# Optimization experiments

Measured on AMD Instinct MI355X. Metric: run time of the kernel, lower is better.

## Reference

```python
import jax, jax.numpy as jnp
import numpy as np


def setup_inputs() -> dict:
    key = jax.random.key(0)
    k_u, k_a, k_b, k_c, k_d = jax.random.split(key, 5)
    B, T, Din, Dout, S = 16, 4096, 256, 256, 256
    return {
        "u": jax.random.normal(k_u, (B, T, Din), dtype=jnp.float32),
        "a_raw": jnp.zeros((S,), dtype=jnp.float32),
        "b": jax.random.normal(k_b, (S, Din), dtype=jnp.float32) * 0.1,
        "c": jax.random.normal(k_c, (Dout, S), dtype=jnp.float32) * 0.1,
        "d": jax.random.normal(k_d, (Dout, Din), dtype=jnp.float32) * 0.1,
    }


def reference(u, a_raw, b, c, d):
    # u: (B, T, Din) -> y: (B, T, Dout)
    # Recurrence: x_t = a * x_{t-1} + b @ u_t ;  y_t = c @ x_t + d @ u_t
    a = jnp.tanh(a_raw)                                  # (S,)
    Bu = jnp.einsum('btd,sd->bts', u, b)                 # input projection, (B,T,S)

    def step(x, bu_t):
        x = x * a + bu_t                                 # diagonal state update
        return x, x

    x0 = jnp.zeros((u.shape[0], a.shape[0]), dtype=u.dtype)
    _, xs = jax.lax.scan(step, x0, jnp.swapaxes(Bu, 0, 1))  # xs: (T,B,S)
    xs = jnp.swapaxes(xs, 0, 1)                              # (B,T,S)

    y = jnp.einsum('bts,os->bto', xs, c) + jnp.einsum('bti,oi->bto', u, d)
    return y  # dropout(p=0.0) is identity
```

## Files before the change

kernel.cpp:

```cpp
#include <hip/hip_runtime.h>

#define DEV __device__ __forceinline__

typedef unsigned short u16;
typedef __attribute__((ext_vector_type(8))) __bf16 bf16x8;
typedef __attribute__((ext_vector_type(4))) float f32x4;
typedef __attribute__((ext_vector_type(8))) unsigned short u16x8;
typedef __attribute__((ext_vector_type(4))) unsigned short u16x4;

static constexpr int NB = 16;
static constexpr int NT = 4096;
static constexpr int NCH = 64;
static constexpr int LCH = 64;

DEV u16 f2bf(float f) {
  unsigned u = __builtin_bit_cast(unsigned, f);
  u += 0x7fffu + ((u >> 16) & 1u);
  return (u16)(u >> 16);
}
DEV float bf2f(u16 h) {
  unsigned u = ((unsigned)h) << 16;
  return __builtin_bit_cast(float, u);
}

DEV void gl_lds16(const void* gp, void* lp) {
  __builtin_amdgcn_global_load_lds(
      (__attribute__((address_space(1))) void*)(void*)gp,
      (__attribute__((address_space(3))) void*)lp, 16, 0, 0);
}

__global__ __launch_bounds__(256) void prep_k(const float* __restrict__ a_raw,
                                              const float* __restrict__ b,
                                              const float* __restrict__ c,
                                              const float* __restrict__ d,
                                              float* __restrict__ af,
                                              u16* __restrict__ wq,
                                              u16* __restrict__ cw) {
  int i = blockIdx.x * 256 + threadIdx.x;
  if (i < 256) af[i] = tanhf(a_raw[i]);
  wq[i] = f2bf(b[i]);
  wq[65536 + i] = f2bf(d[i]);
  cw[i] = f2bf(c[i]);
}

__global__ __launch_bounds__(1024, 4) void gemm1_k(const float* __restrict__ u,
                                                   const u16* __restrict__ wq,
                                                   const float* __restrict__ af,
                                                   u16* __restrict__ bu,
                                                   u16* __restrict__ ud,
                                                   float* __restrict__ carry) {
  __shared__ u16 As[64 * 64];
  __shared__ u16 Ws[512 * 64];
  const int tid = threadIdx.x;
  const int lane = tid & 63;
  const int wid = tid >> 6;
  const int bx = blockIdx.x;
  const size_t row0 = (size_t)bx * 64;

  const int arow = tid >> 4;
  const int ak = (tid & 15) * 4;
  const int abyte = arow * 128 + ((((tid & 15) >> 1) ^ (arow & 7)) * 16) + (tid & 1) * 8;

  const f32x4 zero = {0.f, 0.f, 0.f, 0.f};
  f32x4 acc[4][2];
#pragma unroll
  for (int i = 0; i < 4; ++i) { acc[i][0] = zero; acc[i][1] = zero; }

#pragma unroll
  for (int kt = 0; kt < 4; ++kt) {
    const int kb = kt * 64;
    float4 av = *reinterpret_cast<const float4*>(u + (row0 + arow) * 256 + kb + ak);
#pragma unroll
    for (int r = 0; r < 4; ++r) {
      int wrow = r * 128 + (tid >> 3);
      int sc = (tid & 7) ^ (wrow & 7);
      gl_lds16(wq + (size_t)wrow * 256 + kb + sc * 8,
               (char*)Ws + r * 16384 + wid * 1024);
    }
    u16x4 a4;
    a4[0] = f2bf(av.x); a4[1] = f2bf(av.y); a4[2] = f2bf(av.z); a4[3] = f2bf(av.w);
    *reinterpret_cast<u16x4*>((char*)As + abyte) = a4;
    __syncthreads();
#pragma unroll
    for (int kk = 0; kk < 2; ++kk) {
      const int ks = kk * 4 + (lane >> 4);
      bf16x8 afr[4], bfr[2];
#pragma unroll
      for (int mi = 0; mi < 4; ++mi) {
        int ar = mi * 16 + (lane & 15);
        afr[mi] = *reinterpret_cast<const bf16x8*>(
            (const char*)As + ar * 128 + ((ks ^ (ar & 7)) * 16));
      }
#pragma unroll
      for (int ni = 0; ni < 2; ++ni) {
        int br = wid * 32 + ni * 16 + (lane & 15);
        bfr[ni] = *reinterpret_cast<const bf16x8*>(
            (const char*)Ws + br * 128 + ((ks ^ (br & 7)) * 16));
      }
#pragma unroll
      for (int mi = 0; mi < 4; ++mi)
#pragma unroll
        for (int ni = 0; ni < 2; ++ni)
          acc[mi][ni] = __builtin_amdgcn_mfma_f32_16x16x32_bf16(
              afr[mi], bfr[ni], acc[mi][ni], 0, 0, 0);
    }
    if (kt < 3) __syncthreads();
  }

#pragma unroll
  for (int mi = 0; mi < 4; ++mi) {
    int rl = mi * 16 + (lane >> 4) * 4;
#pragma unroll
    for (int ni = 0; ni < 2; ++ni) {
      int col = wid * 32 + ni * 16 + (lane & 15);
#pragma unroll
      for (int q = 0; q < 4; ++q) {
        size_t R = row0 + rl + q;
        u16 h = f2bf(acc[mi][ni][q]);
        if (wid < 8)
          bu[R * 256 + (((col >> 3) ^ ((int)R & 7)) * 8) + (col & 7)] = h;
        else
          ud[R * 256 + (col - 256)] = h;
      }
    }
  }

  if (wid < 8) {
    const int tb = (lane >> 4) * 4;
#pragma unroll
    for (int ni = 0; ni < 2; ++ni) {
      int col = wid * 32 + ni * 16 + (lane & 15);
      float a = af[col];
      float c2 = a * a, c4 = c2 * c2, c8 = c4 * c4;
      float a12 = c8 * c4;
      float a13 = a12 * a;
      float base = (tb == 0) ? a12 : (tb == 4) ? c8 : (tb == 8) ? c4 : 1.0f;
      float p = base, s = 0.f;
#pragma unroll
      for (int mi = 3; mi >= 0; --mi) {
#pragma unroll
        for (int q = 3; q >= 0; --q) {
          s = fmaf(p, acc[mi][ni][q], s);
          if (q) p *= a;
        }
        if (mi) p *= a13;
      }
      s += __shfl_xor(s, 16, 64);
      s += __shfl_xor(s, 32, 64);
      if ((lane >> 4) == 0) carry[(size_t)bx * 256 + col] = s;
    }
  }
}

__global__ __launch_bounds__(256) void scan2_k(const float* __restrict__ carry,
                                               const float* __restrict__ af,
                                               float* __restrict__ initb) {
  int b = blockIdx.x;
  int s = threadIdx.x;
  float a = af[s];
  float aL = a;
#pragma unroll
  for (int i = 0; i < 6; ++i) aL *= aL;
  float x = 0.f;
  for (int k = 0; k < NCH; ++k) {
    size_t idx = ((size_t)(b * NCH + k)) * 256 + s;
    float cv = carry[idx];
    initb[idx] = x;
    x = fmaf(aL, x, cv);
  }
}

__global__ __launch_bounds__(512, 4) void gemm2_k(const u16* __restrict__ bu,
                                                  const u16* __restrict__ cw,
                                                  const u16* __restrict__ ud,
                                                  const float* __restrict__ af,
                                                  const float* __restrict__ initb,
                                                  float* __restrict__ y) {
  __shared__ u16 XS[128 * 256];
  __shared__ u16 CS[128 * 64];
  const int tid = threadIdx.x;
  const int lane = tid & 63;
  const int wid = tid >> 6;
  const int wr = wid >> 2, wc = wid & 3;
  const int bx = blockIdx.x;
  const int col0 = blockIdx.y * 128;

  const char* src = (const char*)bu + (size_t)bx * 65536;
#pragma unroll
  for (int j = 0; j < 8; ++j)
    gl_lds16(src + j * 8192 + tid * 16, (char*)XS + j * 8192 + wid * 1024);
#pragma unroll
  for (int r = 0; r < 2; ++r) {
    int brow = r * 64 + (tid >> 3);
    int sc = (tid & 7) ^ (brow & 7);
    gl_lds16(cw + (size_t)(col0 + brow) * 256 + 0 + sc * 8,
             (char*)CS + r * 8192 + wid * 1024);
  }
  __syncthreads();

  {
    const int hf = tid >> 8;
    const int s = tid & 255;
    const float a = af[s];
    float x = initb[(size_t)(bx * 2 + hf) * 256 + s];
    const int r0 = hf * 64;
    const int slot = s >> 3;
    const int off = (s & 7);
#pragma unroll 8
    for (int t = 0; t < 64; ++t) {
      int r = r0 + t;
      int bi = r * 256 + ((slot ^ (r & 7)) * 8) + off;
      x = fmaf(a, x, bf2f(XS[bi]));
      XS[bi] = f2bf(x);
    }
  }

  f32x4 acc[4][2];
#pragma unroll
  for (int mi = 0; mi < 4; ++mi) {
    int rlb = wr * 64 + mi * 16 + (lane >> 4) * 4;
#pragma unroll
    for (int ni = 0; ni < 2; ++ni) {
      int col = col0 + wc * 32 + ni * 16 + (lane & 15);
#pragma unroll
      for (int q = 0; q < 4; ++q)
        acc[mi][ni][q] = bf2f(ud[(size_t)(bx * 128 + rlb + q) * 256 + col]);
    }
  }
  __syncthreads();

#pragma unroll
  for (int kt = 0; kt < 4; ++kt) {
#pragma unroll
    for (int kk = 0; kk < 2; ++kk) {
      const int ksl = kk * 4 + (lane >> 4);
      const int ksg = kt * 8 + ksl;
      bf16x8 afr[4], bfr[2];
#pragma unroll
      for (int mi = 0; mi < 4; ++mi) {
        int ar = wr * 64 + mi * 16 + (lane & 15);
        afr[mi] = *reinterpret_cast<const bf16x8*>(&XS[ar * 256 + ((ksg ^ (ar & 7)) * 8)]);
      }
#pragma unroll
      for (int ni = 0; ni < 2; ++ni) {
        int nr = wc * 32 + ni * 16 + (lane & 15);
        bfr[ni] = *reinterpret_cast<const bf16x8*>(&CS[nr * 64 + ((ksl ^ (nr & 7)) * 8)]);
      }
#pragma unroll
      for (int mi = 0; mi < 4; ++mi)
#pragma unroll
        for (int ni = 0; ni < 2; ++ni)
          acc[mi][ni] = __builtin_amdgcn_mfma_f32_16x16x32_bf16(
              afr[mi], bfr[ni], acc[mi][ni], 0, 0, 0);
    }
    if (kt < 3) {
      __syncthreads();
#pragma unroll
      for (int r = 0; r < 2; ++r) {
        int brow = r * 64 + (tid >> 3);
        int sc = (tid & 7) ^ (brow & 7);
        gl_lds16(cw + (size_t)(col0 + brow) * 256 + (kt + 1) * 64 + sc * 8,
                 (char*)CS + r * 8192 + wid * 1024);
      }
      __syncthreads();
    }
  }

#pragma unroll
  for (int mi = 0; mi < 4; ++mi) {
    int rlb = wr * 64 + mi * 16 + (lane >> 4) * 4;
#pragma unroll
    for (int ni = 0; ni < 2; ++ni) {
      int col = col0 + wc * 32 + ni * 16 + (lane & 15);
#pragma unroll
      for (int q = 0; q < 4; ++q)
        y[(size_t)(bx * 128 + rlb + q) * 256 + col] = acc[mi][ni][q];
    }
  }
}

extern "C" void kernel_launch(void* const* d_in, const int* in_sizes, int n_in,
                              void* d_out, int out_size, void* d_ws, size_t ws_size,
                              hipStream_t stream) {
  const float* u = (const float*)d_in[0];
  const float* a_raw = (const float*)d_in[1];
  const float* b = (const float*)d_in[2];
  const float* c = (const float*)d_in[3];
  const float* d = (const float*)d_in[4];
  float* y = (float*)d_out;
  char* ws = (char*)d_ws;

  const size_t MB = 1u << 20;
  float* af = (float*)(ws);
  u16* wq = (u16*)(ws + 65536);
  u16* cw = (u16*)(ws + 65536 + 262144);
  u16* bu = (u16*)(ws + 1 * MB);
  u16* ud = (u16*)(ws + 33 * MB);
  float* carry = (float*)(ws + 65 * MB);
  float* initb = (float*)(ws + 66 * MB);

  prep_k<<<256, 256, 0, stream>>>(a_raw, b, c, d, af, wq, cw);
  gemm1_k<<<1024, 1024, 0, stream>>>(u, wq, af, bu, ud, carry);
  scan2_k<<<16, 256, 0, stream>>>(carry, af, initb);
  gemm2_k<<<dim3(512, 2), 512, 0, stream>>>(bu, cw, ud, af, initb, y);
}
```

Measured before the change: 90.71 us.

## Split gemm1 into 4 column panels per chunk, loading operands directly without LDS

```diff
diff --git a/kernel.cpp b/kernel.cpp
--- a/kernel.cpp
+++ b/kernel.cpp
@@ -27,6 +27,13 @@
   __builtin_amdgcn_global_load_lds(
       (__attribute__((address_space(1))) void*)(void*)gp,
       (__attribute__((address_space(3))) void*)lp, 16, 0, 0);
+}
+
+DEV bf16x8 cvt8(float4 a, float4 b) {
+  u16x8 o;
+  o[0] = f2bf(a.x); o[1] = f2bf(a.y); o[2] = f2bf(a.z); o[3] = f2bf(a.w);
+  o[4] = f2bf(b.x); o[5] = f2bf(b.y); o[6] = f2bf(b.z); o[7] = f2bf(b.w);
+  return __builtin_bit_cast(bf16x8, o);
 }
 
 __global__ __launch_bounds__(256) void prep_k(const float* __restrict__ a_raw,
@@ -43,68 +50,57 @@
   cw[i] = f2bf(c[i]);
 }
 
-__global__ __launch_bounds__(1024, 4) void gemm1_k(const float* __restrict__ u,
-                                                   const u16* __restrict__ wq,
-                                                   const float* __restrict__ af,
-                                                   u16* __restrict__ bu,
-                                                   u16* __restrict__ ud,
-                                                   float* __restrict__ carry) {
-  __shared__ u16 As[64 * 64];
-  __shared__ u16 Ws[512 * 64];
+__global__ __launch_bounds__(256, 3) void gemm1_k(const float* __restrict__ u,
+                                                  const u16* __restrict__ wq,
+                                                  const float* __restrict__ af,
+                                                  u16* __restrict__ bu,
+                                                  u16* __restrict__ ud,
+                                                  float* __restrict__ carry) {
   const int tid = threadIdx.x;
   const int lane = tid & 63;
   const int wid = tid >> 6;
   const int bx = blockIdx.x;
-  const size_t row0 = (size_t)bx * 64;
-
-  const int arow = tid >> 4;
-  const int ak = (tid & 15) * 4;
-  const int abyte = arow * 128 + ((((tid & 15) >> 1) ^ (arow & 7)) * 16) + (tid & 1) * 8;
+  const int chunk = bx >> 2;
+  const int panel = bx & 3;
+  const size_t row0 = (size_t)chunk * 64;
+
+  const int lr = lane & 15;
+  const int lk = (lane >> 4) * 8;
 
   const f32x4 zero = {0.f, 0.f, 0.f, 0.f};
   f32x4 acc[4][2];
 #pragma unroll
   for (int i = 0; i < 4; ++i) { acc[i][0] = zero; acc[i][1] = zero; }
 
+  const float* ubase = u + (row0 + lr) * 256 + lk;
+  const u16* wbase = wq + (size_t)(panel * 128 + wid * 32 + lr) * 256 + lk;
+
 #pragma unroll
   for (int kt = 0; kt < 4; ++kt) {
-    const int kb = kt * 64;
-    float4 av = *reinterpret_cast<const float4*>(u + (row0 + arow) * 256 + kb + ak);
-#pragma unroll
-    for (int r = 0; r < 4; ++r) {
-      int wrow = r * 128 + (tid >> 3);
-      int sc = (tid & 7) ^ (wrow & 7);
-      gl_lds16(wq + (size_t)wrow * 256 + kb + sc * 8,
-               (char*)Ws + r * 16384 + wid * 1024);
-    }
-    u16x4 a4;
-    a4[0] = f2bf(av.x); a4[1] = f2bf(av.y); a4[2] = f2bf(av.z); a4[3] = f2bf(av.w);
-    *reinterpret_cast<u16x4*>((char*)As + abyte) = a4;
-    __syncthreads();
-#pragma unroll
-    for (int kk = 0; kk < 2; ++kk) {
-      const int ks = kk * 4 + (lane >> 4);
-      bf16x8 afr[4], bfr[2];
+#pragma unroll
+    for (int ks = 0; ks < 2; ++ks) {
+      const int k = kt * 64 + ks * 32;
+      float4 a0[4], a1[4];
 #pragma unroll
       for (int mi = 0; mi < 4; ++mi) {
-        int ar = mi * 16 + (lane & 15);
-        afr[mi] = *reinterpret_cast<const bf16x8*>(
-            (const char*)As + ar * 128 + ((ks ^ (ar & 7)) * 16));
-      }
-#pragma unroll
-      for (int ni = 0; ni < 2; ++ni) {
-        int br = wid * 32 + ni * 16 + (lane & 15);
-        bfr[ni] = *reinterpret_cast<const bf16x8*>(
-            (const char*)Ws + br * 128 + ((ks ^ (br & 7)) * 16));
-      }
+        const float* p = ubase + (size_t)mi * 16 * 256 + k;
+        a0[mi] = *reinterpret_cast<const float4*>(p);
+        a1[mi] = *reinterpret_cast<const float4*>(p + 4);
+      }
+      bf16x8 bf[2];
+#pragma unroll
+      for (int ni = 0; ni < 2; ++ni)
+        bf[ni] = *reinterpret_cast<const bf16x8*>(wbase + (size_t)ni * 16 * 256 + k);
+      bf16x8 afr[4];
+#pragma unroll
+      for (int mi = 0; mi < 4; ++mi) afr[mi] = cvt8(a0[mi], a1[mi]);
 #pragma unroll
       for (int mi = 0; mi < 4; ++mi)
 #pragma unroll
         for (int ni = 0; ni < 2; ++ni)
           acc[mi][ni] = __builtin_amdgcn_mfma_f32_16x16x32_bf16(
-              afr[mi], bfr[ni], acc[mi][ni], 0, 0, 0);
-    }
-    if (kt < 3) __syncthreads();
+              afr[mi], bf[ni], acc[mi][ni], 0, 0, 0);
+    }
   }
 
 #pragma unroll
@@ -112,12 +108,12 @@
     int rl = mi * 16 + (lane >> 4) * 4;
 #pragma unroll
     for (int ni = 0; ni < 2; ++ni) {
-      int col = wid * 32 + ni * 16 + (lane & 15);
+      int col = panel * 128 + wid * 32 + ni * 16 + lr;
 #pragma unroll
       for (int q = 0; q < 4; ++q) {
         size_t R = row0 + rl + q;
         u16 h = f2bf(acc[mi][ni][q]);
-        if (wid < 8)
+        if (panel < 2)
           bu[R * 256 + (((col >> 3) ^ ((int)R & 7)) * 8) + (col & 7)] = h;
         else
           ud[R * 256 + (col - 256)] = h;
@@ -125,11 +121,11 @@
     }
   }
 
-  if (wid < 8) {
+  if (panel < 2) {
     const int tb = (lane >> 4) * 4;
 #pragma unroll
     for (int ni = 0; ni < 2; ++ni) {
-      int col = wid * 32 + ni * 16 + (lane & 15);
+      int col = panel * 128 + wid * 32 + ni * 16 + lr;
       float a = af[col];
       float c2 = a * a, c4 = c2 * c2, c8 = c4 * c4;
       float a12 = c8 * c4;
@@ -147,7 +143,7 @@
       }
       s += __shfl_xor(s, 16, 64);
       s += __shfl_xor(s, 32, 64);
-      if ((lane >> 4) == 0) carry[(size_t)bx * 256 + col] = s;
+      if ((lane >> 4) == 0) carry[(size_t)chunk * 256 + col] = s;
     }
   }
 }
@@ -300,7 +296,7 @@
   float* initb = (float*)(ws + 66 * MB);
 
   prep_k<<<256, 256, 0, stream>>>(a_raw, b, c, d, af, wq, cw);
-  gemm1_k<<<1024, 1024, 0, stream>>>(u, wq, af, bu, ud, carry);
+  gemm1_k<<<4096, 256, 0, stream>>>(u, wq, af, bu, ud, carry);
   scan2_k<<<16, 256, 0, stream>>>(carry, af, initb);
   gemm2_k<<<dim3(512, 2), 512, 0, stream>>>(bu, cw, ud, af, initb, y);
 }
```

Result: slower. 200.4 us (+120.9%).

## Convert u to bf16 once and move the D projection into gemm2

Applied to the files above, without the earlier changes.

```diff
diff --git a/kernel.cpp b/kernel.cpp
--- a/kernel.cpp
+++ b/kernel.cpp
@@ -34,73 +34,83 @@
                                               const float* __restrict__ c,
                                               const float* __restrict__ d,
                                               float* __restrict__ af,
-                                              u16* __restrict__ wq,
-                                              u16* __restrict__ cw) {
+                                              u16* __restrict__ bw,
+                                              u16* __restrict__ cw,
+                                              u16* __restrict__ dw) {
   int i = blockIdx.x * 256 + threadIdx.x;
   if (i < 256) af[i] = tanhf(a_raw[i]);
-  wq[i] = f2bf(b[i]);
-  wq[65536 + i] = f2bf(d[i]);
+  bw[i] = f2bf(b[i]);
   cw[i] = f2bf(c[i]);
-}
-
-__global__ __launch_bounds__(1024, 4) void gemm1_k(const float* __restrict__ u,
-                                                   const u16* __restrict__ wq,
-                                                   const float* __restrict__ af,
-                                                   u16* __restrict__ bu,
-                                                   u16* __restrict__ ud,
-                                                   float* __restrict__ carry) {
-  __shared__ u16 As[64 * 64];
-  __shared__ u16 Ws[512 * 64];
+  dw[i] = f2bf(d[i]);
+}
+
+__global__ __launch_bounds__(256) void convu_k(const float* __restrict__ u,
+                                               u16* __restrict__ ub) {
+  size_t i = ((size_t)blockIdx.x * 256 + threadIdx.x) * 8;
+  float4 v0 = *reinterpret_cast<const float4*>(u + i);
+  float4 v1 = *reinterpret_cast<const float4*>(u + i + 4);
+  u16x8 o;
+  o[0] = f2bf(v0.x); o[1] = f2bf(v0.y); o[2] = f2bf(v0.z); o[3] = f2bf(v0.w);
+  o[4] = f2bf(v1.x); o[5] = f2bf(v1.y); o[6] = f2bf(v1.z); o[7] = f2bf(v1.w);
+  *reinterpret_cast<u16x8*>(ub + i) = o;
+}
+
+__global__ __launch_bounds__(256) void gemm1_k(const u16* __restrict__ ubf,
+                                               const u16* __restrict__ bw,
+                                               const float* __restrict__ af,
+                                               u16* __restrict__ bu,
+                                               float* __restrict__ carry) {
+  __shared__ u16 As[128 * 64];
+  __shared__ u16 Bs[128 * 64];
   const int tid = threadIdx.x;
   const int lane = tid & 63;
   const int wid = tid >> 6;
-  const int bx = blockIdx.x;
-  const size_t row0 = (size_t)bx * 64;
-
-  const int arow = tid >> 4;
-  const int ak = (tid & 15) * 4;
-  const int abyte = arow * 128 + ((((tid & 15) >> 1) ^ (arow & 7)) * 16) + (tid & 1) * 8;
+  const int wm = wid >> 1, wn = wid & 1;
+  const int panel = blockIdx.x;
+  const size_t row0 = (size_t)blockIdx.y * 128;
+  const int col0 = panel * 128;
+
+  const int rstg = tid >> 3;
+  const int c16 = tid & 7;
 
   const f32x4 zero = {0.f, 0.f, 0.f, 0.f};
-  f32x4 acc[4][2];
-#pragma unroll
-  for (int i = 0; i < 4; ++i) { acc[i][0] = zero; acc[i][1] = zero; }
+  f32x4 acc[4][4];
+#pragma unroll
+  for (int i = 0; i < 4; ++i)
+#pragma unroll
+    for (int j = 0; j < 4; ++j) acc[i][j] = zero;
 
 #pragma unroll
   for (int kt = 0; kt < 4; ++kt) {
     const int kb = kt * 64;
-    float4 av = *reinterpret_cast<const float4*>(u + (row0 + arow) * 256 + kb + ak);
-#pragma unroll
-    for (int r = 0; r < 4; ++r) {
-      int wrow = r * 128 + (tid >> 3);
-      int sc = (tid & 7) ^ (wrow & 7);
-      gl_lds16(wq + (size_t)wrow * 256 + kb + sc * 8,
-               (char*)Ws + r * 16384 + wid * 1024);
-    }
-    u16x4 a4;
-    a4[0] = f2bf(av.x); a4[1] = f2bf(av.y); a4[2] = f2bf(av.z); a4[3] = f2bf(av.w);
-    *reinterpret_cast<u16x4*>((char*)As + abyte) = a4;
+#pragma unroll
+    for (int j = 0; j < 4; ++j) {
+      int row = j * 32 + rstg;
+      int sc = c16 ^ (row & 7);
+      gl_lds16(ubf + (row0 + row) * 256 + kb + sc * 8,
+               (char*)As + j * 4096 + wid * 1024);
+      gl_lds16(bw + (size_t)(col0 + row) * 256 + kb + sc * 8,
+               (char*)Bs + j * 4096 + wid * 1024);
+    }
     __syncthreads();
 #pragma unroll
     for (int kk = 0; kk < 2; ++kk) {
       const int ks = kk * 4 + (lane >> 4);
-      bf16x8 afr[4], bfr[2];
+      bf16x8 afr[4], bfr[4];
 #pragma unroll
       for (int mi = 0; mi < 4; ++mi) {
-        int ar = mi * 16 + (lane & 15);
-        afr[mi] = *reinterpret_cast<const bf16x8*>(
-            (const char*)As + ar * 128 + ((ks ^ (ar & 7)) * 16));
-      }
-#pragma unroll
-      for (int ni = 0; ni < 2; ++ni) {
-        int br = wid * 32 + ni * 16 + (lane & 15);
-        bfr[ni] = *reinterpret_cast<const bf16x8*>(
-            (const char*)Ws + br * 128 + ((ks ^ (br & 7)) * 16));
+        int ar = wm * 64 + mi * 16 + (lane & 15);
+        afr[mi] = *reinterpret_cast<const bf16x8*>(&As[ar * 64 + (ks ^ (ar & 7)) * 8]);
+      }
+#pragma unroll
+      for (int ni = 0; ni < 4; ++ni) {
+        int br = wn * 64 + ni * 16 + (lane & 15);
+        bfr[ni] = *reinterpret_cast<const bf16x8*>(&Bs[br * 64 + (ks ^ (br & 7)) * 8]);
       }
 #pragma unroll
       for (int mi = 0; mi < 4; ++mi)
 #pragma unroll
-        for (int ni = 0; ni < 2; ++ni)
+        for (int ni = 0; ni < 4; ++ni)
           acc[mi][ni] = __builtin_amdgcn_mfma_f32_16x16x32_bf16(
               afr[mi], bfr[ni], acc[mi][ni], 0, 0, 0);
     }
@@ -109,27 +119,24 @@
 
 #pragma unroll
   for (int mi = 0; mi < 4; ++mi) {
-    int rl = mi * 16 + (lane >> 4) * 4;
-#pragma unroll
-    for (int ni = 0; ni < 2; ++ni) {
-      int col = wid * 32 + ni * 16 + (lane & 15);
+    int rl = wm * 64 + mi * 16 + (lane >> 4) * 4;
+#pragma unroll
+    for (int ni = 0; ni < 4; ++ni) {
+      int col = col0 + wn * 64 + ni * 16 + (lane & 15);
 #pragma unroll
       for (int q = 0; q < 4; ++q) {
         size_t R = row0 + rl + q;
-        u16 h = f2bf(acc[mi][ni][q]);
-        if (wid < 8)
-          bu[R * 256 + (((col >> 3) ^ ((int)R & 7)) * 8) + (col & 7)] = h;
-        else
-          ud[R * 256 + (col - 256)] = h;
-      }
-    }
-  }
-
-  if (wid < 8) {
+        bu[R * 256 + (((col >> 3) ^ ((int)R & 7)) * 8) + (col & 7)] = f2bf(acc[mi][ni][q]);
+      }
+    }
+  }
+
+  {
+    const int chunk = (int)(blockIdx.y) * 2 + wm;
     const int tb = (lane >> 4) * 4;
 #pragma unroll
-    for (int ni = 0; ni < 2; ++ni) {
-      int col = wid * 32 + ni * 16 + (lane & 15);
+    for (int ni = 0; ni < 4; ++ni) {
+      int col = col0 + wn * 64 + ni * 16 + (lane & 15);
       float a = af[col];
       float c2 = a * a, c4 = c2 * c2, c8 = c4 * c4;
       float a12 = c8 * c4;
@@ -147,7 +154,7 @@
       }
       s += __shfl_xor(s, 16, 64);
       s += __shfl_xor(s, 32, 64);
-      if ((lane >> 4) == 0) carry[(size_t)bx * 256 + col] = s;
+      if ((lane >> 4) == 0) carry[(size_t)chunk * 256 + col] = s;
     }
   }
 }
@@ -172,7 +179,8 @@
 
 __global__ __launch_bounds__(512, 4) void gemm2_k(const u16* __restrict__ bu,
                                                   const u16* __restrict__ cw,
-                                                  const u16* __restrict__ ud,
+                                                  const u16* __restrict__ dw,
+                                                  const u16* __restrict__ ubf,
                                                   const float* __restrict__ af,
                                                   const float* __restrict__ initb,
                                                   float* __restrict__ y) {
@@ -182,8 +190,8 @@
   const int lane = tid & 63;
   const int wid = tid >> 6;
   const int wr = wid >> 2, wc = wid & 3;
-  const int bx = blockIdx.x;
-  const int col0 = blockIdx.y * 128;
+  const int bx = blockIdx.y;
+  const int col0 = blockIdx.x * 128;
 
   const char* src = (const char*)bu + (size_t)bx * 65536;
 #pragma unroll
@@ -216,17 +224,9 @@
   }
 
   f32x4 acc[4][2];
-#pragma unroll
-  for (int mi = 0; mi < 4; ++mi) {
-    int rlb = wr * 64 + mi * 16 + (lane >> 4) * 4;
-#pragma unroll
-    for (int ni = 0; ni < 2; ++ni) {
-      int col = col0 + wc * 32 + ni * 16 + (lane & 15);
-#pragma unroll
-      for (int q = 0; q < 4; ++q)
-        acc[mi][ni][q] = bf2f(ud[(size_t)(bx * 128 + rlb + q) * 256 + col]);
-    }
-  }
+  const f32x4 zero = {0.f, 0.f, 0.f, 0.f};
+#pragma unroll
+  for (int mi = 0; mi < 4; ++mi) { acc[mi][0] = zero; acc[mi][1] = zero; }
   __syncthreads();
 
 #pragma unroll
@@ -263,6 +263,48 @@
                  (char*)CS + r * 8192 + wid * 1024);
       }
       __syncthreads();
+    }
+  }
+
+#pragma unroll
+  for (int kt = 0; kt < 4; ++kt) {
+    __syncthreads();
+#pragma unroll
+    for (int j = 0; j < 2; ++j) {
+      int row = j * 64 + (tid >> 3);
+      int sc = (tid & 7) ^ (row & 7);
+      gl_lds16(ubf + ((size_t)bx * 128 + row) * 256 + kt * 64 + sc * 8,
+               (char*)XS + j * 8192 + wid * 1024);
+    }
+#pragma unroll
+    for (int r = 0; r < 2; ++r) {
+      int brow = r * 64 + (tid >> 3);
+      int sc = (tid & 7) ^ (brow & 7);
+      gl_lds16(dw + (size_t)(col0 + brow) * 256 + kt * 64 + sc * 8,
+               (char*)CS + r * 8192 + wid * 1024);
+    }
+    __syncthreads();
+#pragma unroll
+    for (int kk = 0; kk < 2; ++kk) {
+      const int ksl = kk * 4 + (lane >> 4);
+      bf16x8 afr[4], bfr[2];
+#pragma unroll
+      for (int mi = 0; mi < 4; ++mi) {
+        int ar = wr * 64 + mi * 16 + (lane & 15);
+        afr[mi] = *reinterpret_cast<const bf16x8*>(
+            (const char*)XS + ar * 128 + ((ksl ^ (ar & 7)) * 16));
+      }
+#pragma unroll
+      for (int ni = 0; ni < 2; ++ni) {
+        int nr = wc * 32 + ni * 16 + (lane & 15);
+        bfr[ni] = *reinterpret_cast<const bf16x8*>(&CS[nr * 64 + ((ksl ^ (nr & 7)) * 8)]);
+      }
+#pragma unroll
+      for (int mi = 0; mi < 4; ++mi)
+#pragma unroll
+        for (int ni = 0; ni < 2; ++ni)
+          acc[mi][ni] = __builtin_amdgcn_mfma_f32_16x16x32_bf16(
+              afr[mi], bfr[ni], acc[mi][ni], 0, 0, 0);
     }
   }
 
@@ -292,15 +334,17 @@
 
   const size_t MB = 1u << 20;
   float* af = (float*)(ws);
-  u16* wq = (u16*)(ws + 65536);
-  u16* cw = (u16*)(ws + 65536 + 262144);
-  u16* bu = (u16*)(ws + 1 * MB);
-  u16* ud = (u16*)(ws + 33 * MB);
+  u16* bw = (u16*)(ws + 4096);
+  u16* cw = (u16*)(ws + 4096 + 131072);
+  u16* dw = (u16*)(ws + 4096 + 2 * 131072);
+  u16* ubf = (u16*)(ws + 1 * MB);
+  u16* bu = (u16*)(ws + 33 * MB);
   float* carry = (float*)(ws + 65 * MB);
   float* initb = (float*)(ws + 66 * MB);
 
-  prep_k<<<256, 256, 0, stream>>>(a_raw, b, c, d, af, wq, cw);
-  gemm1_k<<<1024, 1024, 0, stream>>>(u, wq, af, bu, ud, carry);
+  prep_k<<<256, 256, 0, stream>>>(a_raw, b, c, d, af, bw, cw, dw);
+  convu_k<<<8192, 256, 0, stream>>>(u, ubf);
+  gemm1_k<<<dim3(2, 512), 256, 0, stream>>>(ubf, bw, af, bu, carry);
   scan2_k<<<16, 256, 0, stream>>>(carry, af, initb);
-  gemm2_k<<<dim3(512, 2), 512, 0, stream>>>(bu, cw, ud, af, initb, y);
-}
+  gemm2_k<<<dim3(2, 512), 512, 0, stream>>>(bu, cw, dw, ubf, af, initb, y);
+}
```

Result: slower. 93.03 us (+2.6%).
